# Kernel tuning notes

Measured on AMD Instinct MI355X. Metric: run time of the kernel, lower is better.

Reference implementation:

```python
import jax, jax.numpy as jnp
import numpy as np

PATCH = 14
N_HEAD = 8
TOP_K = 2

def _ln(x, g, b, eps=1e-5):
    m = jnp.mean(x, -1, keepdims=True)
    v = jnp.var(x, -1, keepdims=True)
    return (x - m) * jax.lax.rsqrt(v + eps) * g + b

def _mha(x, wq, bq, wk, bk, wv, bv, wo, bo):
    B, S, D = x.shape
    hd = D // N_HEAD
    def split(t):
        return t.reshape(B, S, N_HEAD, hd).transpose(0, 2, 1, 3)
    q = split(x @ wq + bq)
    k = split(x @ wk + bk)
    v = split(x @ wv + bv)
    scores = jnp.einsum('bhqd,bhkd->bhqk', q, k) / jnp.sqrt(jnp.asarray(hd, x.dtype))
    attn = jax.nn.softmax(scores, -1)  # [B,H,S,S]
    out = jnp.einsum('bhqk,bhkd->bhqd', attn, v).transpose(0, 2, 1, 3).reshape(B, S, D)
    return out @ wo + bo, attn

def _moe(x, rw, rb, w1, b1, w2, b2):
    # dense-compute-all-experts-then-mask, matching SparseMoE.forward
    B, S, D = x.shape
    E = rw.shape[1]
    probs = jax.nn.softmax(x @ rw + rb, -1)           # [B,S,E]
    topv, topi = jax.lax.top_k(probs, TOP_K)          # [B,S,K]
    oh = jax.nn.one_hot(topi, E, dtype=x.dtype)       # [B,S,K,E]
    mask = jnp.sum(oh * topv[..., None], -2)          # [B,S,E] top-k gates, zeros elsewhere
    h = jax.nn.gelu(jnp.einsum('bsd,edh->besh', x, w1) + b1[None, :, None, :], approximate=False)
    outs = jnp.einsum('besh,ehd->besd', h, w2) + b2[None, :, None, :]
    out = jnp.einsum('besd,bse->bsd', outs, mask)     # masked sum over experts
    # load-balancing auxiliary loss
    frac = jnp.mean(jnp.sum(oh, -2).reshape(-1, E), 0)
    imp = jnp.mean(probs.reshape(-1, E), 0)
    loss = E * jnp.sum(frac * imp)
    return out, loss

def setup_inputs():
    key = jax.random.key(0)
    B, C, IMG = 32, 3, 224
    D, E, HID = 512, 8, 2048
    S = (IMG // PATCH) ** 2
    PD = C * PATCH * PATCH
    ks = iter(jax.random.split(key, 64))
    def w(shape, fan):
        return jax.random.normal(next(ks), shape, jnp.float32) / np.sqrt(fan).astype(np.float32)
    def moe_params():
        return dict(rw=w((D, E), D), rb=jnp.zeros(E), w1=w((E, D, HID), D), b1=jnp.zeros((E, HID)), w2=w((E, HID, D), HID), b2=jnp.zeros((E, D)))
    m1 = moe_params(); m2 = moe_params()
    return dict(
        x=jax.random.normal(next(ks), (B, C, IMG, IMG), jnp.float32),
        pe_w=w((PD, D), PD), pe_b=jnp.zeros(D),
        pos=w((1, S, D), D),
        ln1_g=jnp.ones(D), ln1_b=jnp.zeros(D),
        ln2_g=jnp.ones(D), ln2_b=jnp.zeros(D),
        ln3_g=jnp.ones(D), ln3_b=jnp.zeros(D),
        wq=w((D, D), D), bq=jnp.zeros(D), wk=w((D, D), D), bk=jnp.zeros(D),
        wv=w((D, D), D), bv=jnp.zeros(D), wo=w((D, D), D), bo=jnp.zeros(D),
        m1_rw=m1['rw'], m1_rb=m1['rb'], m1_w1=m1['w1'], m1_b1=m1['b1'], m1_w2=m1['w2'], m1_b2=m1['b2'],
        m2_rw=m2['rw'], m2_rb=m2['rb'], m2_w1=m2['w1'], m2_b1=m2['b1'], m2_w2=m2['w2'], m2_b2=m2['b2'],
        cls_w=w((D, D), D), cls_b=jnp.zeros(D))

def reference(x, pe_w, pe_b, pos, ln1_g, ln1_b, ln2_g, ln2_b, ln3_g, ln3_b, wq, bq, wk, bk, wv, bv, wo, bo, m1_rw, m1_rb, m1_w1, m1_b1, m1_w2, m1_b2, m2_rw, m2_rb, m2_w1, m2_b1, m2_w2, m2_b2, cls_w, cls_b):
    B, C, H, W = x.shape
    h = H // PATCH
    # einops 'b c (h p1) (w p2) -> b (h w) (p1 p2 c)'
    patches = x.reshape(B, C, h, PATCH, h, PATCH).transpose(0, 2, 4, 3, 5, 1).reshape(B, h * h, PATCH * PATCH * C)
    e = patches @ pe_w + pe_b + pos
    sa, attn = _mha(_ln(e, ln1_g, ln1_b), wq, bq, wk, bk, wv, bv, wo, bo)
    e = e + sa  # dropout is identity at eval
    o1, l1 = _moe(_ln(e, ln2_g, ln2_b), m1_rw, m1_rb, m1_w1, m1_b1, m1_w2, m1_b2)
    o2, l2 = _moe(_ln(o1, ln3_g, ln3_b), m2_rw, m2_rb, m2_w1, m2_b1, m2_w2, m2_b2)
    fv = jnp.mean(o2, 1)
    logits = fv @ cls_w + cls_b
    attn_w = jax.nn.softmax(jnp.mean(attn, 1), -1)  # mean over heads then re-softmax, as in source
    return logits, fv, l1 + l2, attn_w
```

## Files before the change

kernel.cpp:

```cpp
#include <hip/hip_runtime.h>
#include <hip/hip_bf16.h>

using bf16 = __hip_bfloat16;
typedef unsigned short u16;
typedef __attribute__((ext_vector_type(8))) short short8;
typedef __attribute__((ext_vector_type(4))) float f32x4;

#define DEVFN __device__ __forceinline__

DEVFN u16 f2bu(float v) { return __builtin_bit_cast(u16, __float2bfloat16(v)); }
DEVFN float us2f(u16 u) { union { unsigned int i; float f; } x; x.i = ((unsigned int)u) << 16; return x.f; }
DEVFN void unp8(uint4 u, float* f) {
  f[0]=us2f(u.x & 0xffffu); f[1]=us2f(u.x >> 16);
  f[2]=us2f(u.y & 0xffffu); f[3]=us2f(u.y >> 16);
  f[4]=us2f(u.z & 0xffffu); f[5]=us2f(u.z >> 16);
  f[6]=us2f(u.w & 0xffffu); f[7]=us2f(u.w >> 16);
}

DEVFN f32x4 mfma16(short8 a, short8 b, f32x4 c) {
  return __builtin_amdgcn_mfma_f32_16x16x32_bf16(a, b, c, 0, 0, 0);
}

DEVFN void gl16(const u16* g, u16* l) {
  __builtin_amdgcn_global_load_lds((const __attribute__((address_space(1))) void*)g,
                                   (__attribute__((address_space(3))) void*)l, 16, 0, 0);
}

static constexpr size_t OF_PATCH = 0;
static constexpr size_t OF_E     = 4816896;
static constexpr size_t OF_XN    = 9011200;
static constexpr size_t OF_Q     = 13205504;
static constexpr size_t OF_FV    = 38371328;
static constexpr size_t OF_GATES = 38387712;
static constexpr size_t OF_IMPS  = 38404096;
static constexpr size_t OF_CNT   = 38404104;
static constexpr size_t OF_BASE  = 38404112;
static constexpr size_t OF_CURS  = 38404120;
static constexpr size_t OF_LOSS  = 38404128;
static constexpr size_t OF_TOPI  = 38404136;
static constexpr size_t OF_RPOS  = 38420520;
static constexpr size_t OF_RLIST = 38436904;
static constexpr size_t OF_Q16   = 13205504;
static constexpr size_t OF_K16   = 15302656;
static constexpr size_t OF_VT    = 17399808;
static constexpr size_t OF_CTX16 = 19496960;
static constexpr size_t OF_PET   = 21594112;
static constexpr size_t OF_WQT   = 21757952;
static constexpr size_t OF_WKT   = 21889024;
static constexpr size_t OF_WVT   = 22020096;
static constexpr size_t OF_WOT   = 22151168;
static constexpr size_t OF_O1    = 29982720;
static constexpr size_t OF_O2    = 34177024;

__global__ __launch_bounds__(256) void k_patchify(const float* __restrict__ x, u16* __restrict__ XP) {
  int idx = blockIdx.x * 256 + threadIdx.x;
  if (idx >= 8192 * 640) return;
  int row = idx / 640, j = idx - row * 640;
  u16 v = 0;
  if (j < 588) {
    int b = row >> 8, s = row & 255;
    int hh = s >> 4, ww = s & 15;
    int c = j % 3, tt = j / 3;
    int p2 = tt % 14, p1 = tt / 14;
    int src = ((b * 3 + c) * 224 + hh * 14 + p1) * 224 + (ww * 14 + p2);
    v = f2bu(x[src]);
  }
  XP[idx] = v;
}

__global__ __launch_bounds__(256) void k_wcvtd(const float* __restrict__ W, u16* __restrict__ WT, int K, int KP)
{
  __shared__ float s[32][33];
  const int t = threadIdx.x;
  const int tx = t & 31, ty = t >> 5;
  const int k0 = blockIdx.x * 32, n0 = blockIdx.y * 32;
#pragma unroll
  for (int i = 0; i < 4; i++) {
    int kk = k0 + ty + i * 8;
    s[ty + i * 8][tx] = (kk < K) ? W[(size_t)kk * 512 + n0 + tx] : 0.f;
  }
  __syncthreads();
#pragma unroll
  for (int i = 0; i < 4; i++) WT[(size_t)(n0 + ty + i * 8) * KP + k0 + tx] = f2bu(s[tx][ty + i * 8]);
}

__global__ __launch_bounds__(256) void k_wcvt(const float* __restrict__ W, u16* __restrict__ Wt, int K, int N)
{
  __shared__ float s[32][33];
  const int t = threadIdx.x;
  const int tx = t & 31, ty = t >> 5;
  const int k0 = blockIdx.x * 32, n0 = blockIdx.y * 32;
  const size_t es = (size_t)K * N;
  const float* We = W + (size_t)blockIdx.z * es;
  u16* Wte = Wt + (size_t)blockIdx.z * es;
#pragma unroll
  for (int i = 0; i < 4; i++) s[ty + i * 8][tx] = We[(size_t)(k0 + ty + i * 8) * N + n0 + tx];
  __syncthreads();
#pragma unroll
  for (int i = 0; i < 4; i++) Wte[(size_t)(n0 + ty + i * 8) * K + k0 + tx] = f2bu(s[tx][ty + i * 8]);
}

#define WAIT_VM8  asm volatile("s_waitcnt vmcnt(8)" ::: "memory")
#define WAIT_VM0  asm volatile("s_waitcnt vmcnt(0)" ::: "memory")
#define WAIT_LG0  asm volatile("s_waitcnt lgkmcnt(0)" ::: "memory")
#define BARRIER   __builtin_amdgcn_s_barrier()

DEVFN void mma_stage(const u16* const agp[4], const u16* const bgp[4],
                     u16* Asb, u16* Bsb, int k0, int widx)
{
#pragma unroll
  for (int q = 0; q < 4; q++) {
    gl16(agp[q] + k0, Asb + (q * 256 + widx * 64) * 8);
    gl16(bgp[q] + k0, Bsb + (q * 256 + widx * 64) * 8);
  }
}

DEVFN void mma_step(f32x4 acc[4][4], const u16* As, const u16* Bs,
                    int wm, int wn, int ml, int kq)
{
  __builtin_amdgcn_s_setprio(1);
#pragma unroll
  for (int ks = 0; ks < 2; ks++) {
    const int c = ks * 4 + kq;
    short8 af[4], bf[4];
#pragma unroll
    for (int i = 0; i < 4; i++) {
      const int row = wm + i * 16 + ml;
      af[i] = *(const short8*)&As[row * 64 + ((c ^ (row & 7)) << 3)];
    }
#pragma unroll
    for (int j = 0; j < 4; j++) {
      const int row = wn + j * 16 + ml;
      bf[j] = *(const short8*)&Bs[row * 64 + ((c ^ (row & 7)) << 3)];
    }
#pragma unroll
    for (int i = 0; i < 4; i++)
#pragma unroll
      for (int j = 0; j < 4; j++) acc[i][j] = mfma16(af[i], bf[j], acc[i][j]);
  }
  __builtin_amdgcn_s_setprio(0);
}

DEVFN void mma_loop(f32x4 acc[4][4], const u16* const agp[4], const u16* const bgp[4],
                    u16* SB, int K, int wm, int wn, int ml, int kq, int widx)
{
  u16* As0 = SB;          u16* Bs0 = SB + 8192;
  u16* As1 = SB + 16384;  u16* Bs1 = SB + 24576;
  const int NT = K >> 6;
  mma_stage(agp, bgp, As0, Bs0, 0, widx);
  mma_stage(agp, bgp, As1, Bs1, 64, widx);
  int k = 128;
  for (int t = 0; t + 2 < NT; t += 2) {
    WAIT_VM8;
    BARRIER;
    mma_step(acc, As0, Bs0, wm, wn, ml, kq);
    WAIT_LG0;
    BARRIER;
    mma_stage(agp, bgp, As0, Bs0, k, widx);
    WAIT_VM8;
    BARRIER;
    mma_step(acc, As1, Bs1, wm, wn, ml, kq);
    WAIT_LG0;
    BARRIER;
    mma_stage(agp, bgp, As1, Bs1, k + 64, widx);
    k += 128;
  }
  WAIT_VM8;
  BARRIER;
  mma_step(acc, As0, Bs0, wm, wn, ml, kq);
  WAIT_VM0;
  BARRIER;
  mma_step(acc, As1, Bs1, wm, wn, ml, kq);
}

DEVFN void ep_xpose(float* ep, const f32x4* ai, int kq, int ml, int er, int ec, float* v)
{
#pragma unroll
  for (int j = 0; j < 4; j++)
#pragma unroll
    for (int r = 0; r < 4; r++)
      ep[(kq * 4 + r) * 68 + j * 16 + ml] = ai[j][r];
  __syncthreads();
#pragma unroll
  for (int u = 0; u < 4; u++) {
    float4 f = *(const float4*)&ep[er * 68 + ec + u * 4];
    v[u * 4 + 0] = f.x; v[u * 4 + 1] = f.y; v[u * 4 + 2] = f.z; v[u * 4 + 3] = f.w;
  }
  __syncthreads();
}

template<int MODE>
__global__ __launch_bounds__(256) void k_bgemm(const u16* __restrict__ A, const u16* __restrict__ BT,
    const float* __restrict__ bias, float* __restrict__ Cf, u16* __restrict__ O16,
    const float* __restrict__ pos, int K)
{
  const int m0 = blockIdx.y * 128, n0 = blockIdx.x * 128;
  __shared__ alignas(16) u16 SB[32768];
  const int t = threadIdx.x;
  const int widx = t >> 6, lane = t & 63;
  const int wm = (widx & 1) * 64, wn = (widx >> 1) * 64;
  const int ml = lane & 15, kq = lane >> 4;
  const u16* agp[4]; const u16* bgp[4];
#pragma unroll
  for (int q = 0; q < 4; q++) {
    const int slot = q * 256 + t;
    const int row = slot >> 3;
    const int c = (slot & 7) ^ (row & 7);
    agp[q] = A + (size_t)(m0 + row) * K + c * 8;
    bgp[q] = BT + (size_t)(n0 + row) * K + c * 8;
  }
  f32x4 acc[4][4];
#pragma unroll
  for (int i = 0; i < 4; i++)
#pragma unroll
    for (int j = 0; j < 4; j++) acc[i][j] = (f32x4){0.f, 0.f, 0.f, 0.f};
  mma_loop(acc, agp, bgp, SB, K, wm, wn, ml, kq, widx);

  if (MODE == 3) {
#pragma unroll
    for (int j = 0; j < 4; j++) {
      const int n = n0 + wn + j * 16 + ml;
      const float bv = bias[n];
      const int h = n >> 6, d = n & 63;
#pragma unroll
      for (int i = 0; i < 4; i++) {
        const int mb = m0 + wm + i * 16 + kq * 4;
        const int b = mb >> 8, s0 = mb & 255;
        ushort4 w4;
        w4.x = f2bu(acc[i][j][0] + bv); w4.y = f2bu(acc[i][j][1] + bv);
        w4.z = f2bu(acc[i][j][2] + bv); w4.w = f2bu(acc[i][j][3] + bv);
        *(ushort4*)(O16 + ((size_t)(b * 8 + h) * 64 + d) * 256 + s0) = w4;
      }
    }
    return;
  }

  __syncthreads();
  float* ep = (float*)SB + widx * (16 * 68);
  const int er = lane >> 2, ec = (lane & 3) * 16;
  const int gn = n0 + wn + ec;
  float bb[16];
#pragma unroll
  for (int u = 0; u < 4; u++) {
    float4 f = *(const float4*)(bias + gn + u * 4);
    bb[u*4]=f.x; bb[u*4+1]=f.y; bb[u*4+2]=f.z; bb[u*4+3]=f.w;
  }
#pragma unroll
  for (int i = 0; i < 4; i++) {
    float v[16];
    ep_xpose(ep, acc[i], kq, ml, er, ec, v);
    const int gm = m0 + wm + i * 16 + er;
    if (MODE == 0) {
      const float* pr = pos + (size_t)(gm & 255) * 512 + gn;
      float* cp = Cf + (size_t)gm * 512 + gn;
#pragma unroll
      for (int u = 0; u < 4; u++) {
        float4 p = *(const float4*)(pr + u * 4);
        float4 o = {v[u*4]+bb[u*4]+p.x, v[u*4+1]+bb[u*4+1]+p.y, v[u*4+2]+bb[u*4+2]+p.z, v[u*4+3]+bb[u*4+3]+p.w};
        *(float4*)(cp + u * 4) = o;
      }
    } else if (MODE == 1) {
      union { u16 h[16]; uint4 q2[2]; } pk;
#pragma unroll
      for (int u = 0; u < 16; u++) pk.h[u] = f2bu(v[u] + bb[u]);
      u16* hp = O16 + (size_t)gm * 512 + gn;
      *(uint4*)hp = pk.q2[0]; *(uint4*)(hp + 8) = pk.q2[1];
    } else {
      float* cp = Cf + (size_t)gm * 512 + gn;
#pragma unroll
      for (int u = 0; u < 4; u++) {
        float4 oldv = *(const float4*)(cp + u * 4);
        float4 o = {oldv.x+v[u*4]+bb[u*4], oldv.y+v[u*4+1]+bb[u*4+1], oldv.z+v[u*4+2]+bb[u*4+2], oldv.w+v[u*4+3]+bb[u*4+3]};
        *(float4*)(cp + u * 4) = o;
      }
    }
  }
}

__global__ __launch_bounds__(256) void k_ln(const float* __restrict__ X, float* __restrict__ Y,
    u16* __restrict__ YB16, const float* __restrict__ g, const float* __restrict__ b)
{
  __shared__ float red[256];
  const int row = blockIdx.x;
  const int t = threadIdx.x;
  const float* xr = X + (size_t)row * 512;
  float x0 = xr[t], x1 = xr[t + 256];
  red[t] = x0 + x1;
  __syncthreads();
  for (int s = 128; s > 0; s >>= 1) { if (t < s) red[t] += red[t + s]; __syncthreads(); }
  float mean = red[0] * (1.f / 512.f);
  __syncthreads();
  float d0 = x0 - mean, d1 = x1 - mean;
  red[t] = d0 * d0 + d1 * d1;
  __syncthreads();
  for (int s = 128; s > 0; s >>= 1) { if (t < s) red[t] += red[t + s]; __syncthreads(); }
  float rs = 1.f / sqrtf(red[0] * (1.f / 512.f) + 1e-5f);
  float y0 = d0 * rs * g[t]       + b[t];
  float y1 = d1 * rs * g[t + 256] + b[t + 256];
  float* yr = Y + (size_t)row * 512;
  yr[t] = y0; yr[t + 256] = y1;
  u16* br16 = YB16 + (size_t)row * 512;
  br16[t] = f2bu(y0); br16[t + 256] = f2bu(y1);
}

__global__ __launch_bounds__(256) void k_fattn(const u16* __restrict__ Q16, const u16* __restrict__ K16,
    const u16* __restrict__ VT, u16* __restrict__ CTX16, u16* __restrict__ Pg)
{
  __shared__ u16 P[64 * 264];
  __shared__ u16 kv[64 * 136];
  const int t = threadIdx.x;
  const int qt = blockIdx.x, h = blockIdx.y, b = blockIdx.z;
  const int q0 = qt * 64;
  const int lane = t & 63, w = t >> 6;
  const int ml = lane & 15, kq = lane >> 4;
  const int srow = t >> 2, spart = t & 3;

  const size_t tokq = (size_t)(b * 256 + q0 + w * 16 + ml);
  short8 aq0 = *(const short8*)(Q16 + tokq * 512 + h * 64 + kq * 8);
  short8 aq1 = *(const short8*)(Q16 + tokq * 512 + h * 64 + 32 + kq * 8);

  f32x4 sacc[16];
#pragma unroll
  for (int i = 0; i < 16; i++) sacc[i] = (f32x4){0.f, 0.f, 0.f, 0.f};

  for (int kc = 0; kc < 4; kc++) {
    __syncthreads();
    {
      const u16* src = K16 + (size_t)(b * 256 + kc * 64 + srow) * 512 + h * 64 + spart * 16;
      uint4 v0 = *(const uint4*)src;
      uint4 v1 = *(const uint4*)(src + 8);
      *(uint4*)&kv[srow * 72 + spart * 16] = v0;
      *(uint4*)&kv[srow * 72 + spart * 16 + 8] = v1;
    }
    __syncthreads();
#pragma unroll
    for (int kt = 0; kt < 4; kt++) {
      short8 bk0 = *(const short8*)&kv[(kt * 16 + ml) * 72 + kq * 8];
      short8 bk1 = *(const short8*)&kv[(kt * 16 + ml) * 72 + 32 + kq * 8];
      sacc[kc * 4 + kt] = mfma16(aq0, bk0, sacc[kc * 4 + kt]);
      sacc[kc * 4 + kt] = mfma16(aq1, bk1, sacc[kc * 4 + kt]);
    }
  }

#pragma unroll
  for (int r = 0; r < 4; r++) {
    float v[16];
    float mx = -1e30f;
#pragma unroll
    for (int tl = 0; tl < 16; tl++) { v[tl] = sacc[tl][r] * 0.125f; mx = fmaxf(mx, v[tl]); }
#pragma unroll
    for (int mk = 1; mk < 16; mk <<= 1) mx = fmaxf(mx, __shfl_xor(mx, mk, 64));
    float sum = 0.f;
#pragma unroll
    for (int tl = 0; tl < 16; tl++) { v[tl] = __expf(v[tl] - mx); sum += v[tl]; }
#pragma unroll
    for (int mk = 1; mk < 16; mk <<= 1) sum += __shfl_xor(sum, mk, 64);
    float inv = 1.f / sum;
    const int qrow = w * 16 + kq * 4 + r;
#pragma unroll
    for (int tl = 0; tl < 16; tl++) P[qrow * 264 + tl * 16 + ml] = f2bu(v[tl] * inv);
  }
  __syncthreads();

  {
    const int row_l = w * 16 + (lane >> 2);
    const int cp0 = (lane & 3) * 64;
    u16* dst = Pg + ((size_t)(b * 8 + h) * 256 + q0 + row_l) * 256 + cp0;
    const u16* srcl = &P[row_l * 264 + cp0];
#pragma unroll
    for (int i = 0; i < 8; i++) *(uint4*)(dst + i * 8) = *(const uint4*)(srcl + i * 8);
  }

  f32x4 oacc[4];
#pragma unroll
  for (int j = 0; j < 4; j++) oacc[j] = (f32x4){0.f, 0.f, 0.f, 0.f};
  for (int half = 0; half < 2; half++) {
    __syncthreads();
    {
      const u16* src = VT + ((size_t)(b * 8 + h) * 64 + srow) * 256 + half * 128 + spart * 32;
#pragma unroll
      for (int i = 0; i < 4; i++)
        *(uint4*)&kv[srow * 136 + spart * 32 + i * 8] = *(const uint4*)(src + i * 8);
    }
    __syncthreads();
#pragma unroll
    for (int st = 0; st < 4; st++) {
      short8 ap = *(const short8*)&P[(w * 16 + ml) * 264 + half * 128 + st * 32 + kq * 8];
#pragma unroll
      for (int j = 0; j < 4; j++) {
        short8 bv = *(const short8*)&kv[(j * 16 + ml) * 136 + st * 32 + kq * 8];
        oacc[j] = mfma16(ap, bv, oacc[j]);
      }
    }
  }

#pragma unroll
  for (int j = 0; j < 4; j++) {
    const int d = h * 64 + j * 16 + ml;
#pragma unroll
    for (int r = 0; r < 4; r++) {
      const int tok = b * 256 + q0 + w * 16 + kq * 4 + r;
      CTX16[(size_t)tok * 512 + d] = f2bu(oacc[j][r]);
    }
  }
}

__global__ __launch_bounds__(256) void k_attnw(const u16* __restrict__ Pg, float* __restrict__ AW)
{
  const int t = threadIdx.x;
  const int qt = blockIdx.x, b = blockIdx.y;
  const int row = t >> 4, seg = t & 15;
  const int q = qt * 16 + row;
  float vals[16];
#pragma unroll
  for (int i = 0; i < 16; i++) vals[i] = 0.f;
#pragma unroll
  for (int h = 0; h < 8; h++) {
    const u16* src = Pg + ((size_t)(b * 8 + h) * 256 + q) * 256 + seg * 16;
    uint4 u0 = *(const uint4*)src;
    uint4 u1 = *(const uint4*)(src + 8);
    float f0[8], f1[8];
    unp8(u0, f0); unp8(u1, f1);
#pragma unroll
    for (int i = 0; i < 8; i++) { vals[i] += f0[i]; vals[8 + i] += f1[i]; }
  }
  float vmax = -1e30f;
#pragma unroll
  for (int i = 0; i < 16; i++) { vals[i] *= 0.125f; vmax = fmaxf(vmax, vals[i]); }
#pragma unroll
  for (int mk = 1; mk < 16; mk <<= 1) vmax = fmaxf(vmax, __shfl_xor(vmax, mk, 64));
  float ssum = 0.f;
#pragma unroll
  for (int i = 0; i < 16; i++) { vals[i] = __expf(vals[i] - vmax); ssum += vals[i]; }
#pragma unroll
  for (int mk = 1; mk < 16; mk <<= 1) ssum += __shfl_xor(ssum, mk, 64);
  float inv = 1.f / ssum;
  float* orow = AW + (size_t)(b * 256 + q) * 256 + seg * 16;
#pragma unroll
  for (int i = 0; i < 16; i++) orow[i] = vals[i] * inv;
}

DEVFN int rwidx(int k, int e) { return k * 8 + e + (k >> 6) * 4; }

__global__ __launch_bounds__(256) void k_router(const float* __restrict__ XNp, const float* __restrict__ rw,
    const float* __restrict__ rb, float* __restrict__ gates, int* __restrict__ topi,
    int* __restrict__ cnt, float* __restrict__ imps)
{
  __shared__ float rws[4128];
  const int t = threadIdx.x;
  for (int i = t; i < 4096; i += 256) rws[rwidx(i >> 3, i & 7)] = rw[i];
  __syncthreads();
  const int w = t >> 6, l = t & 63;
  const int e = l & 7, ch = l >> 3;
  float impAcc = 0.f; int cntAcc = 0;
  const int row0 = blockIdx.x * 32 + w * 8;
  for (int r = 0; r < 8; r++) {
    const int row = row0 + r;
    const float* xr = XNp + (size_t)row * 512 + ch * 64;
    float s = 0.f;
#pragma unroll 8
    for (int j = 0; j < 64; j++) s = fmaf(xr[j], rws[rwidx(ch * 64 + j, e)], s);
    s += __shfl_xor(s, 8, 64);
    s += __shfl_xor(s, 16, 64);
    s += __shfl_xor(s, 32, 64);
    s += rb[e];
    float p[8];
#pragma unroll
    for (int i = 0; i < 8; i++) p[i] = __shfl(s, (l & 56) | i, 64);
    float mx = p[0];
#pragma unroll
    for (int i = 1; i < 8; i++) mx = fmaxf(mx, p[i]);
    float sum = 0.f;
#pragma unroll
    for (int i = 0; i < 8; i++) { p[i] = __expf(p[i] - mx); sum += p[i]; }
    float inv = 1.f / sum;
#pragma unroll
    for (int i = 0; i < 8; i++) p[i] *= inv;
    int t0 = 0; float v0 = p[0];
#pragma unroll
    for (int i = 1; i < 8; i++) if (p[i] > v0) { v0 = p[i]; t0 = i; }
    int t1 = -1; float v1 = -1.f;
#pragma unroll
    for (int i = 0; i < 8; i++) if (i != t0 && p[i] > v1) { v1 = p[i]; t1 = i; }
    if (l < 8) { impAcc += p[e]; cntAcc += (t0 == e) + (t1 == e); }
    if (l == 0) {
      gates[(size_t)row * 2] = v0; gates[(size_t)row * 2 + 1] = v1;
      topi[(size_t)row * 2] = t0;  topi[(size_t)row * 2 + 1] = t1;
    }
  }
  if (l < 8) { atomicAdd(&imps[e], impAcc); atomicAdd(&cnt[e], cntAcc); }
}

__global__ void k_scan(const int* __restrict__ cnt, int* __restrict__ basep, int* __restrict__ curs) {
  if (threadIdx.x == 0) {
    int a = 0;
    for (int e = 0; e < 8; e++) { basep[e] = a; a += cnt[e]; }
  }
  if (threadIdx.x < 8) curs[threadIdx.x] = 0;
}

__global__ __launch_bounds__(256) void k_scatter(const int* __restrict__ topi, const int* __restrict__ basep,
    int* __restrict__ cursor, int* __restrict__ rowlist, int* __restrict__ rowpos)
{
  __shared__ int lcnt[8], lbase[8];
  const int t = threadIdx.x;
  if (t < 8) lcnt[t] = 0;
  __syncthreads();
  const int token = blockIdx.x * 256 + t;
  const int e0 = topi[token * 2], e1 = topi[token * 2 + 1];
  const int p0 = atomicAdd(&lcnt[e0], 1);
  const int p1 = atomicAdd(&lcnt[e1], 1);
  __syncthreads();
  if (t < 8) lbase[t] = atomicAdd(&cursor[t], lcnt[t]);
  __syncthreads();
  const int pos0 = basep[e0] + lbase[e0] + p0;
  const int pos1 = basep[e1] + lbase[e1] + p1;
  rowlist[pos0] = token; rowlist[pos1] = token;
  rowpos[token * 2] = pos0; rowpos[token * 2 + 1] = pos1;
}

__global__ void k_loss(const int* __restrict__ cnt, const float* __restrict__ imps,
                       float* __restrict__ lossws, float* __restrict__ out, int phase) {
  if (threadIdx.x == 0 && blockIdx.x == 0) {
    float s = 0.f;
    for (int e = 0; e < 8; e++) s += ((float)cnt[e]) * imps[e];
    s *= 8.f / (8192.f * 8192.f);
    if (phase == 0) *lossws = s;
    else out[0] = *lossws + s;
  }
}

__global__ __launch_bounds__(256) void k_mg1(const u16* __restrict__ XNB, const u16* __restrict__ W1T,
    const float* __restrict__ B1, u16* __restrict__ H,
    const int* __restrict__ rowlist, const int* __restrict__ basep, const int* __restrict__ cntp)
{
  const int e = blockIdx.z;
  const int cnt = cntp[e];
  const int m0 = blockIdx.y * 128;
  if (m0 >= cnt) return;
  const int base = basep[e];
  const int n0 = blockIdx.x * 128;
  __shared__ alignas(16) u16 SB[32768];
  __shared__ int rl[128];
  const int t = threadIdx.x;
  if (t < 128) rl[t] = rowlist[base + min(m0 + t, cnt - 1)];
  __syncthreads();
  const int widx = t >> 6, lane = t & 63;
  const int wm = (widx & 1) * 64, wn = (widx >> 1) * 64;
  const int ml = lane & 15, kq = lane >> 4;
  const u16* wt = W1T + (size_t)e * (2048 * 512);
  const u16* agp[4]; const u16* bgp[4];
#pragma unroll
  for (int q = 0; q < 4; q++) {
    const int slot = q * 256 + t;
    const int row = slot >> 3;
    const int c = (slot & 7) ^ (row & 7);
    agp[q] = XNB + (size_t)rl[row] * 512 + c * 8;
    bgp[q] = wt + (size_t)(n0 + row) * 512 + c * 8;
  }
  f32x4 acc[4][4];
#pragma unroll
  for (int i = 0; i < 4; i++)
#pragma unroll
    for (int j = 0; j < 4; j++) acc[i][j] = (f32x4){0.f, 0.f, 0.f, 0.f};
  mma_loop(acc, agp, bgp, SB, 512, wm, wn, ml, kq, widx);

  __syncthreads();
  float* ep = (float*)SB + widx * (16 * 68);
  const int er = lane >> 2, ec = (lane & 3) * 16;
  const int gn = n0 + wn + ec;
  float bb[16];
#pragma unroll
  for (int u = 0; u < 4; u++) {
    float4 f = *(const float4*)(B1 + e * 2048 + gn + u * 4);
    bb[u*4]=f.x; bb[u*4+1]=f.y; bb[u*4+2]=f.z; bb[u*4+3]=f.w;
  }
#pragma unroll
  for (int i = 0; i < 4; i++) {
    float v[16];
    ep_xpose(ep, acc[i], kq, ml, er, ec, v);
    const int lr = wm + i * 16 + er;
    if (m0 + lr < cnt) {
      union { u16 h[16]; uint4 q2[2]; } pk;
#pragma unroll
      for (int u = 0; u < 16; u++) {
        float vv = v[u] + bb[u];
        float g = 0.5f * vv * (1.f + erff(vv * 0.70710678118654752f));
        pk.h[u] = f2bu(g);
      }
      u16* hp = H + (size_t)(base + m0 + lr) * 2048 + gn;
      *(uint4*)hp = pk.q2[0]; *(uint4*)(hp + 8) = pk.q2[1];
    }
  }
}

__global__ __launch_bounds__(256) void k_mg2(const u16* __restrict__ H, const u16* __restrict__ W2T,
    const float* __restrict__ B2, float* __restrict__ YB,
    const int* __restrict__ basep, const int* __restrict__ cntp)
{
  const int e = blockIdx.z;
  const int cnt = cntp[e];
  const int m0 = blockIdx.y * 128;
  if (m0 >= cnt) return;
  const int base = basep[e];
  const int n0 = blockIdx.x * 128;
  __shared__ alignas(16) u16 SB[32768];
  const int t = threadIdx.x;
  const int widx = t >> 6, lane = t & 63;
  const int wm = (widx & 1) * 64, wn = (widx >> 1) * 64;
  const int ml = lane & 15, kq = lane >> 4;
  const u16* wt = W2T + (size_t)e * (512 * 2048);
  const u16* agp[4]; const u16* bgp[4];
#pragma unroll
  for (int q = 0; q < 4; q++) {
    const int slot = q * 256 + t;
    const int row = slot >> 3;
    const int c = (slot & 7) ^ (row & 7);
    const int gr = min(base + m0 + row, 16383);
    agp[q] = H + (size_t)gr * 2048 + c * 8;
    bgp[q] = wt + (size_t)(n0 + row) * 2048 + c * 8;
  }
  f32x4 acc[4][4];
#pragma unroll
  for (int i = 0; i < 4; i++)
#pragma unroll
    for (int j = 0; j < 4; j++) acc[i][j] = (f32x4){0.f, 0.f, 0.f, 0.f};
  mma_loop(acc, agp, bgp, SB, 2048, wm, wn, ml, kq, widx);

  __syncthreads();
  float* ep = (float*)SB + widx * (16 * 68);
  const int er = lane >> 2, ec = (lane & 3) * 16;
  const int gn = n0 + wn + ec;
  float bb[16];
#pragma unroll
  for (int u = 0; u < 4; u++) {
    float4 f = *(const float4*)(B2 + e * 512 + gn + u * 4);
    bb[u*4]=f.x; bb[u*4+1]=f.y; bb[u*4+2]=f.z; bb[u*4+3]=f.w;
  }
#pragma unroll
  for (int i = 0; i < 4; i++) {
    float v[16];
    ep_xpose(ep, acc[i], kq, ml, er, ec, v);
    const int lr = wm + i * 16 + er;
    if (m0 + lr < cnt) {
      float* yp = YB + (size_t)(base + m0 + lr) * 512 + gn;
#pragma unroll
      for (int u = 0; u < 4; u++) {
        float4 o = {v[u*4]+bb[u*4], v[u*4+1]+bb[u*4+1], v[u*4+2]+bb[u*4+2], v[u*4+3]+bb[u*4+3]};
        *(float4*)(yp + u * 4) = o;
      }
    }
  }
}

__global__ __launch_bounds__(256) void k_combine(const float* __restrict__ YB, const float* __restrict__ gates,
    const int* __restrict__ rowpos, float* __restrict__ OUT)
{
  const int idx = blockIdx.x * 256 + threadIdx.x;
  const int row = idx >> 9, d = idx & 511;
  const float g0 = gates[row * 2], g1 = gates[row * 2 + 1];
  const int r0 = rowpos[row * 2], r1 = rowpos[row * 2 + 1];
  OUT[idx] = g0 * YB[(size_t)r0 * 512 + d] + g1 * YB[(size_t)r1 * 512 + d];
}

__global__ __launch_bounds__(256) void k_fv(const float* __restrict__ O2, float* __restrict__ FVp, float* __restrict__ outv) {
  const int idx = blockIdx.x * 256 + threadIdx.x;
  const int b = idx >> 9, d = idx & 511;
  const float* p = O2 + (size_t)b * 131072 + d;
  float s = 0.f;
  for (int i = 0; i < 256; i++) s += p[i * 512];
  s *= (1.f / 256.f);
  FVp[idx] = s;
  outv[idx] = s;
}

__global__ __launch_bounds__(256) void k_cls(const float* __restrict__ FVp, const float* __restrict__ W,
    const float* __restrict__ bias, float* __restrict__ outl) {
  const int idx = blockIdx.x * 256 + threadIdx.x;
  const int b = idx >> 9, n = idx & 511;
  const float* f = FVp + (size_t)b * 512;
  float s = 0.f;
  for (int d = 0; d < 512; d++) s = fmaf(f[d], W[(size_t)d * 512 + n], s);
  s += bias[n];
  outl[idx] = s;
}

extern "C" void kernel_launch(void* const* d_in, const int* in_sizes, int n_in,
                              void* d_out, int out_size, void* d_ws, size_t ws_size,
                              hipStream_t stream)
{
  (void)in_sizes; (void)n_in; (void)out_size; (void)ws_size;
  const float* x    = (const float*)d_in[0];
  const float* pe_w = (const float*)d_in[1];
  const float* pe_b = (const float*)d_in[2];
  const float* pos  = (const float*)d_in[3];
  const float* ln1g = (const float*)d_in[4];
  const float* ln1b = (const float*)d_in[5];
  const float* lng[2] = {(const float*)d_in[6], (const float*)d_in[8]};
  const float* lnb[2] = {(const float*)d_in[7], (const float*)d_in[9]};
  const float* wq = (const float*)d_in[10]; const float* bq = (const float*)d_in[11];
  const float* wk = (const float*)d_in[12]; const float* bk = (const float*)d_in[13];
  const float* wv = (const float*)d_in[14]; const float* bv = (const float*)d_in[15];
  const float* wo = (const float*)d_in[16]; const float* bo = (const float*)d_in[17];
  const float* m_rw[2] = {(const float*)d_in[18], (const float*)d_in[24]};
  const float* m_rb[2] = {(const float*)d_in[19], (const float*)d_in[25]};
  const float* m_w1[2] = {(const float*)d_in[20], (const float*)d_in[26]};
  const float* m_b1[2] = {(const float*)d_in[21], (const float*)d_in[27]};
  const float* m_w2[2] = {(const float*)d_in[22], (const float*)d_in[28]};
  const float* m_b2[2] = {(const float*)d_in[23], (const float*)d_in[29]};
  const float* cls_w = (const float*)d_in[30];
  const float* cls_b = (const float*)d_in[31];

  float* ws = (float*)d_ws;
  u16* XP    = (u16*)(ws + OF_PATCH);
  float* ebuf = ws + OF_E;
  float* xn   = ws + OF_XN;
  u16* Q16   = (u16*)(ws + OF_Q16);
  u16* K16   = (u16*)(ws + OF_K16);
  u16* VTb   = (u16*)(ws + OF_VT);
  u16* ctx16 = (u16*)(ws + OF_CTX16);
  u16* peT   = (u16*)(ws + OF_PET);
  u16* wqT   = (u16*)(ws + OF_WQT);
  u16* wkT   = (u16*)(ws + OF_WKT);
  u16* wvT   = (u16*)(ws + OF_WVT);
  u16* woT   = (u16*)(ws + OF_WOT);
  u16* Pgb   = (u16*)(ws + OF_O1);
  float* o1   = ws + OF_O1;
  float* o2   = ws + OF_O2;
  float* fv   = ws + OF_FV;
  float* gates = ws + OF_GATES;
  float* imps  = ws + OF_IMPS;
  int* cnt    = (int*)(ws + OF_CNT);
  int* basep  = (int*)(ws + OF_BASE);
  int* curs   = (int*)(ws + OF_CURS);
  float* lossws = ws + OF_LOSS;
  int* topi   = (int*)(ws + OF_TOPI);
  int* rowpos = (int*)(ws + OF_RPOS);
  int* rowlist= (int*)(ws + OF_RLIST);
  u16* Hbuf  = (u16*)(ws + OF_Q);
  float* YB  = ws + OF_PATCH;
  u16* XNB   = (u16*)(ws + OF_PATCH);
  u16* W1T   = (u16*)(ws + OF_O1);
  u16* W2T   = (u16*)(ws + OF_O2);

  float* out = (float*)d_out;
  float* out_logits = out;
  float* out_fv     = out + 16384;
  float* out_loss   = out + 32768;
  float* out_attnw  = out + 32769;

  k_wcvtd<<<dim3(20, 16), 256, 0, stream>>>(pe_w, peT, 588, 640);
  k_wcvtd<<<dim3(16, 16), 256, 0, stream>>>(wq, wqT, 512, 512);
  k_wcvtd<<<dim3(16, 16), 256, 0, stream>>>(wk, wkT, 512, 512);
  k_wcvtd<<<dim3(16, 16), 256, 0, stream>>>(wv, wvT, 512, 512);
  k_wcvtd<<<dim3(16, 16), 256, 0, stream>>>(wo, woT, 512, 512);

  k_patchify<<<20480, 256, 0, stream>>>(x, XP);
  k_bgemm<0><<<dim3(4, 64), 256, 0, stream>>>(XP, peT, pe_b, ebuf, nullptr, pos, 640);
  k_ln<<<8192, 256, 0, stream>>>(ebuf, xn, XNB, ln1g, ln1b);
  k_bgemm<1><<<dim3(4, 64), 256, 0, stream>>>(XNB, wqT, bq, nullptr, Q16, nullptr, 512);
  k_bgemm<1><<<dim3(4, 64), 256, 0, stream>>>(XNB, wkT, bk, nullptr, K16, nullptr, 512);
  k_bgemm<3><<<dim3(4, 64), 256, 0, stream>>>(XNB, wvT, bv, nullptr, VTb, nullptr, 512);
  k_fattn<<<dim3(4, 8, 32), 256, 0, stream>>>(Q16, K16, VTb, ctx16, Pgb);
  k_attnw<<<dim3(16, 32), 256, 0, stream>>>(Pgb, out_attnw);
  k_bgemm<2><<<dim3(4, 64), 256, 0, stream>>>(ctx16, woT, bo, ebuf, nullptr, nullptr, 512);

  const float* moe_in[2] = {ebuf, o1};
  float* moe_out[2] = {o1, o2};
  for (int mi = 0; mi < 2; mi++) {
    hipMemsetAsync(imps, 0, 64, stream);
    k_ln<<<8192, 256, 0, stream>>>(moe_in[mi], xn, XNB, lng[mi], lnb[mi]);
    k_wcvt<<<dim3(16, 64, 8), 256, 0, stream>>>(m_w1[mi], W1T, 512, 2048);
    k_wcvt<<<dim3(64, 16, 8), 256, 0, stream>>>(m_w2[mi], W2T, 2048, 512);
    k_router<<<256, 256, 0, stream>>>(xn, m_rw[mi], m_rb[mi], gates, topi, cnt, imps);
    k_scan<<<1, 64, 0, stream>>>(cnt, basep, curs);
    k_scatter<<<32, 256, 0, stream>>>(topi, basep, curs, rowlist, rowpos);
    k_loss<<<1, 64, 0, stream>>>(cnt, imps, lossws, out_loss, mi);
    k_mg1<<<dim3(16, 64, 8), 256, 0, stream>>>(XNB, W1T, m_b1[mi], Hbuf, rowlist, basep, cnt);
    k_mg2<<<dim3(4, 64, 8), 256, 0, stream>>>(Hbuf, W2T, m_b2[mi], YB, basep, cnt);
    k_combine<<<16384, 256, 0, stream>>>(YB, gates, rowpos, moe_out[mi]);
  }
  k_fv<<<64, 256, 0, stream>>>(o2, fv, out_fv);
  k_cls<<<64, 256, 0, stream>>>(fv, cls_w, cls_b, out_logits);
}
```

Before: 861.6 us.

## Simplify GEMM double-buffer loop, drop epilogue barriers, use fast GELU approximation

Replaces the two-deep prefetch main loop with a simpler one-ahead loop: it issues the next tile's global-to-LDS loads, computes the current tile, then waits for all loads and synchronises once per tile. It removes the __syncthreads in the per-wave epilogue transpose, relying on each wave writing and reading only its own scratch region. It swaps erff in the MoE GELU for an Abramowitz-Stegun polynomial with a hardware reciprocal and fast exp. These trade prefetch depth for fewer barriers, and accept lower erf accuracy and possible missing intra-wave LDS ordering.

```diff
diff --git a/kernel.cpp b/kernel.cpp
--- a/kernel.cpp
+++ b/kernel.cpp
@@ -24,6 +24,20 @@
 DEVFN void gl16(const u16* g, u16* l) {
   __builtin_amdgcn_global_load_lds((const __attribute__((address_space(1))) void*)g,
                                    (__attribute__((address_space(3))) void*)l, 16, 0, 0);
+}
+
+DEVFN float gelu_f(float v) {
+  float z = v * 0.70710678118654752f;
+  float a = __builtin_fabsf(z);
+  float t = __builtin_amdgcn_rcpf(__builtin_fmaf(0.3275911f, a, 1.0f));
+  float q = __builtin_fmaf(t, 1.061405429f, -1.453152027f);
+  q = __builtin_fmaf(t, q, 1.421413741f);
+  q = __builtin_fmaf(t, q, -0.284496736f);
+  q = __builtin_fmaf(t, q, 0.254829592f);
+  float e = __expf(-z * z);
+  float y = __builtin_fmaf(-q * t, e, 1.0f);
+  float er = __builtin_copysignf(y, z);
+  return 0.5f * v * (1.0f + er);
 }
 
 static constexpr size_t OF_PATCH = 0;
@@ -100,9 +114,7 @@
   for (int i = 0; i < 4; i++) Wte[(size_t)(n0 + ty + i * 8) * K + k0 + tx] = f2bu(s[tx][ty + i * 8]);
 }
 
-#define WAIT_VM8  asm volatile("s_waitcnt vmcnt(8)" ::: "memory")
 #define WAIT_VM0  asm volatile("s_waitcnt vmcnt(0)" ::: "memory")
-#define WAIT_LG0  asm volatile("s_waitcnt lgkmcnt(0)" ::: "memory")
 #define BARRIER   __builtin_amdgcn_s_barrier()
 
 DEVFN void mma_stage(const u16* const agp[4], const u16* const bgp[4],
@@ -144,33 +156,22 @@
 DEVFN void mma_loop(f32x4 acc[4][4], const u16* const agp[4], const u16* const bgp[4],
                     u16* SB, int K, int wm, int wn, int ml, int kq, int widx)
 {
-  u16* As0 = SB;          u16* Bs0 = SB + 8192;
-  u16* As1 = SB + 16384;  u16* Bs1 = SB + 24576;
   const int NT = K >> 6;
-  mma_stage(agp, bgp, As0, Bs0, 0, widx);
-  mma_stage(agp, bgp, As1, Bs1, 64, widx);
-  int k = 128;
-  for (int t = 0; t + 2 < NT; t += 2) {
-    WAIT_VM8;
-    BARRIER;
-    mma_step(acc, As0, Bs0, wm, wn, ml, kq);
-    WAIT_LG0;
-    BARRIER;
-    mma_stage(agp, bgp, As0, Bs0, k, widx);
-    WAIT_VM8;
-    BARRIER;
-    mma_step(acc, As1, Bs1, wm, wn, ml, kq);
-    WAIT_LG0;
-    BARRIER;
-    mma_stage(agp, bgp, As1, Bs1, k + 64, widx);
-    k += 128;
-  }
-  WAIT_VM8;
-  BARRIER;
-  mma_step(acc, As0, Bs0, wm, wn, ml, kq);
+  mma_stage(agp, bgp, SB, SB + 8192, 0, widx);
   WAIT_VM0;
   BARRIER;
-  mma_step(acc, As1, Bs1, wm, wn, ml, kq);
+  int cur = 0;
+  for (int t = 0; t + 1 < NT; ++t) {
+    u16* Nx = SB + ((cur ^ 1) << 14);
+    mma_stage(agp, bgp, Nx, Nx + 8192, (t + 1) << 6, widx);
+    u16* Cu = SB + (cur << 14);
+    mma_step(acc, Cu, Cu + 8192, wm, wn, ml, kq);
+    WAIT_VM0;
+    BARRIER;
+    cur ^= 1;
+  }
+  u16* Cu = SB + (cur << 14);
+  mma_step(acc, Cu, Cu + 8192, wm, wn, ml, kq);
 }
 
 DEVFN void ep_xpose(float* ep, const f32x4* ai, int kq, int ml, int er, int ec, float* v)
@@ -180,13 +181,11 @@
 #pragma unroll
     for (int r = 0; r < 4; r++)
       ep[(kq * 4 + r) * 68 + j * 16 + ml] = ai[j][r];
-  __syncthreads();
 #pragma unroll
   for (int u = 0; u < 4; u++) {
     float4 f = *(const float4*)&ep[er * 68 + ec + u * 4];
     v[u * 4 + 0] = f.x; v[u * 4 + 1] = f.y; v[u * 4 + 2] = f.z; v[u * 4 + 3] = f.w;
   }
-  __syncthreads();
 }
 
 template<int MODE>
@@ -583,11 +582,7 @@
     if (m0 + lr < cnt) {
       union { u16 h[16]; uint4 q2[2]; } pk;
 #pragma unroll
-      for (int u = 0; u < 16; u++) {
-        float vv = v[u] + bb[u];
-        float g = 0.5f * vv * (1.f + erff(vv * 0.70710678118654752f));
-        pk.h[u] = f2bu(g);
-      }
+      for (int u = 0; u < 16; u++) pk.h[u] = f2bu(gelu_f(v[u] + bb[u]));
       u16* hp = H + (size_t)(base + m0 + lr) * 2048 + gn;
       *(uint4*)hp = pk.q2[0]; *(uint4*)(hp + 8) = pk.q2[1];
     }
```

Result: faster. 817.0 us (-5.2%).
